# Kernel tuning notes

Hardware: AMD Instinct MI355X
Metric: run time of the kernel (lower is better)

## Reference

```python
import jax, jax.numpy as jnp
import numpy as np

T = 512   # timesteps (also used as batch-index count for packing)
B = 512   # batch (must equal T for this module's packing to be consistent)
D = 300   # state_dim
H = 128   # hidden_state_dim
E = 64    # embedding_dim
EGO = 12  # ego_state slice fed to the LSTMCell


def setup_inputs() -> dict:
    key = jax.random.key(0)
    ks = jax.random.split(key, 10)
    k = float(1.0 / np.sqrt(H))  # torch LSTMCell uniform init bound
    state = jax.random.normal(ks[0], (T, B, D), dtype=jnp.float32)
    hidden_state = jax.random.normal(ks[1], (B, H), dtype=jnp.float32) * 0.1
    cell_state = jax.random.normal(ks[2], (B, H), dtype=jnp.float32) * 0.1
    len_sequence = jax.random.randint(ks[3], (T,), 1, T + 1, dtype=jnp.int64 if jax.config.jax_enable_x64 else jnp.int32)
    W_ih = jax.random.uniform(ks[4], (4 * H, EGO), minval=-k, maxval=k, dtype=jnp.float32)
    W_hh = jax.random.uniform(ks[5], (4 * H, H), minval=-k, maxval=k, dtype=jnp.float32)
    b_ih = jax.random.uniform(ks[6], (4 * H,), minval=-k, maxval=k, dtype=jnp.float32)
    b_hh = jax.random.uniform(ks[7], (4 * H,), minval=-k, maxval=k, dtype=jnp.float32)
    W_emb = jax.random.normal(ks[8], (E, D + H), dtype=jnp.float32) * 0.05
    b_emb = jnp.zeros((E,), dtype=jnp.float32)
    return dict(state=state, hidden_state=hidden_state, cell_state=cell_state,
                len_sequence=len_sequence, W_ih=W_ih, W_hh=W_hh, b_ih=b_ih,
                b_hh=b_hh, W_emb=W_emb, b_emb=b_emb)


def _pack_indices(L):
    # tmp_output[t][:L[t]] concat over t -> flat indices into [T*B, .] (row-major t,b)
    idx_rnn = np.concatenate([t * B + np.arange(int(L[t])) for t in range(T)]) if T else np.zeros((0,), np.int32)
    # state.permute(1,0,2)[b][:L[b]] concat over b -> flat indices into [B*T, .] (row-major b,t)
    idx_state = np.concatenate([b * T + np.arange(int(L[b])) for b in range(B)]) if B else np.zeros((0,), np.int32)
    return jnp.asarray(idx_rnn, jnp.int32), jnp.asarray(idx_state, jnp.int32)


def _lstm_scan(x_seq, h0, c0, W_ih, W_hh, b_ih, b_hh):
    # torch.nn.LSTMCell math; gate order [i, f, g, o]
    def step(carry, x_t):
        h, c = carry
        gates = x_t @ W_ih.T + b_ih + h @ W_hh.T + b_hh  # [B, 4H]
        i, f, g, o = jnp.split(gates, 4, axis=-1)
        c_new = jax.nn.sigmoid(f) * c + jax.nn.sigmoid(i) * jnp.tanh(g)
        h_new = jax.nn.sigmoid(o) * jnp.tanh(c_new)
        return (h_new, c_new), h_new
    _, hs = jax.lax.scan(step, (h0, c0), x_seq)
    return hs  # [T, B, H]


def reference(state, hidden_state, cell_state, len_sequence, W_ih, W_hh, b_ih, b_hh, W_emb, b_emb):
    L = np.asarray(len_sequence)
    idx_rnn, idx_state = _pack_indices(L)
    rnn_input = state[:, :, :EGO]                               # [T, B, 12]
    hs = _lstm_scan(rnn_input, hidden_state, cell_state, W_ih, W_hh, b_ih, b_hh)  # [T, B, H]
    rnn_packed = hs.reshape(T * B, H)[idx_rnn]                  # [N, H]
    state_packed = jnp.transpose(state, (1, 0, 2)).reshape(B * T, D)[idx_state]  # [N, D]
    feats = jnp.concatenate([state_packed, rnn_packed], axis=1)  # [N, D+H]
    return feats @ W_emb.T + b_emb                               # [N, E]
```

## Files before the change

### kernel.cpp

```cpp
#include <hip/hip_runtime.h>
#include <hip/hip_fp16.h>

#define T_ 512
#define B_ 512
#define D_ 300
#define H_ 128
#define E_ 64
#define EGO_ 12
#define DH_ 428
#define BD_ 153600

typedef __attribute__((ext_vector_type(2))) _Float16 half2_t;
typedef __attribute__((ext_vector_type(8))) _Float16 half8_t;
typedef __attribute__((ext_vector_type(4))) float float4_t;

__device__ __forceinline__ unsigned pack2(float a, float b) {
  __half2 h = __floats2half2_rn(a, b);
  return __builtin_bit_cast(unsigned, h);
}
__device__ __forceinline__ half8_t h8(uint4 u) {
  return __builtin_bit_cast(half8_t, u);
}
__device__ __forceinline__ float sigm(float x) {
  float e = __builtin_amdgcn_exp2f(-1.4426950408889634f * x);
  return __builtin_amdgcn_rcpf(1.0f + e);
}
__device__ __forceinline__ float tanh_(float x) {
  float e = __builtin_amdgcn_exp2f(2.8853900817779268f * x);
  return 1.0f - 2.0f * __builtin_amdgcn_rcpf(1.0f + e);
}

__global__ void prefix_k(const int* __restrict__ L, int* __restrict__ pfx) {
  __shared__ int s[T_];
  int t = threadIdx.x;
  s[t] = L[t];
  __syncthreads();
  for (int off = 1; off < T_; off <<= 1) {
    int v = 0;
    if (t >= off) v = s[t - off];
    __syncthreads();
    s[t] += v;
    __syncthreads();
  }
  if (t == 0) pfx[0] = 0;
  pfx[t + 1] = s[t];
}

#define WS_ 84
__launch_bounds__(256, 1)
__global__ void scan_k(const float* __restrict__ state,
                       const float* __restrict__ h0,
                       const float* __restrict__ c0,
                       const int* __restrict__ lens,
                       const float* __restrict__ W_ih,
                       const float* __restrict__ W_hh,
                       const float* __restrict__ b_ih,
                       const float* __restrict__ b_hh,
                       const float* __restrict__ W_emb,
                       const float* __restrict__ b_emb,
                       const int* __restrict__ pfx,
                       float* __restrict__ out) {
  __shared__ __align__(16) unsigned hb[2][16][WS_];
  __shared__ int pfx_s[T_], len_s[T_];

  const int tid  = threadIdx.x;
  const int lane = tid & 63;
  const int w    = tid >> 6;
  const int n16  = lane & 15;
  const int quad = lane >> 4;
  const int b0   = blockIdx.x * 2;

  uint4 bfr[4][2][5];
  float bias[4][2];
#pragma unroll
  for (int c = 0; c < 4; ++c) {
#pragma unroll
    for (int p = 0; p < 2; ++p) {
      const int g = c * 128 + w * 32 + 2 * n16 + p;
      bias[c][p] = b_ih[g] + b_hh[g];
#pragma unroll
      for (int s = 0; s < 5; ++s) {
        unsigned pk[4];
#pragma unroll
        for (int pp = 0; pp < 4; ++pp) {
          const int k0 = s * 32 + quad * 8 + 2 * pp;
          float f0 = 0.f, f1 = 0.f;
          if (k0 < 128) { f0 = W_hh[g * H_ + k0]; f1 = W_hh[g * H_ + k0 + 1]; }
          else if (k0 < 140) {
            f0 = W_ih[g * EGO_ + (k0 - 128)];
            if (k0 + 1 < 140) f1 = W_ih[g * EGO_ + (k0 - 127)];
          }
          pk[pp] = pack2(f0, f1);
        }
        bfr[c][p][s] = make_uint4(pk[0], pk[1], pk[2], pk[3]);
      }
    }
  }
  uint4 efr[4];
  const int e_ = w * 16 + n16;
  const float bemb = b_emb[e_];
#pragma unroll
  for (int s = 0; s < 4; ++s) {
    unsigned pk[4];
#pragma unroll
    for (int pp = 0; pp < 4; ++pp) {
      const int k0 = s * 32 + quad * 8 + 2 * pp;
      pk[pp] = pack2(W_emb[e_ * DH_ + D_ + k0], W_emb[e_ * DH_ + D_ + k0 + 1]);
    }
    efr[s] = make_uint4(pk[0], pk[1], pk[2], pk[3]);
  }

  for (int i = tid; i < 2 * 16 * WS_; i += 256) ((unsigned*)hb)[i] = 0u;
  for (int i = tid; i < T_; i += 256) { pfx_s[i] = pfx[i]; len_s[i] = lens[i]; }
  __syncthreads();
  if (tid < 128) {
    const int r = tid >> 6, d = tid & 63;
    float2 v = ((const float2*)(h0 + (b0 + r) * H_))[d];
    hb[0][4 * r][d] = pack2(v.x, v.y);
  }
  float2 xheld = make_float2(0.f, 0.f);
  if (tid >= 16 && tid < 28) {
    const int j = tid - 16, row = j / 6, jj = j % 6;
    float2 v = ((const float2*)(state + (b0 + row) * D_))[jj];
    hb[0][4 * row][64 + jj] = pack2(v.x, v.y);
    xheld = ((const float2*)(state + BD_ + (b0 + row) * D_))[jj];
  }
  float cst[2] = {0.f, 0.f};
  if (quad < 2) {
#pragma unroll
    for (int p = 0; p < 2; ++p)
      cst[p] = c0[(b0 + quad) * H_ + w * 32 + 2 * n16 + p];
  }
  __syncthreads();

#pragma unroll 1
  for (int t = 0; t < T_; ++t) {
    const int pb = t & 1;
    float2 xnew = xheld;
    if (tid >= 16 && tid < 28) {
      const int j = tid - 16, row = j / 6, jj = j % 6;
      const int ttx = (t + 2 < T_) ? t + 2 : T_ - 1;
      xnew = ((const float2*)(state + (size_t)ttx * BD_ + (b0 + row) * D_))[jj];
    }

    uint4 a[5];
#pragma unroll
    for (int s = 0; s < 5; ++s)
      a[s] = *(const uint4*)(&hb[pb][n16][s * 16 + quad * 4]);

    if (t > 0) {
      float4_t ea = (float4_t){bemb, bemb, bemb, bemb};
#pragma unroll
      for (int s = 0; s < 4; ++s)
        ea = __builtin_amdgcn_mfma_f32_16x16x32_f16(h8(a[s]), h8(efr[s]), ea, 0, 0, 0);
      if (quad < 2) {
        const int Lt = len_s[t - 1];
        if (b0 + quad < Lt)
          out[((size_t)pfx_s[t - 1] + b0 + quad) * E_ + e_] = ea[0];
      }
    }

    float4_t acc[4][2];
#pragma unroll
    for (int c = 0; c < 4; ++c)
#pragma unroll
      for (int p = 0; p < 2; ++p)
        acc[c][p] = (float4_t){bias[c][p], bias[c][p], bias[c][p], bias[c][p]};
#pragma unroll
    for (int s = 0; s < 5; ++s) {
      const half8_t ah = h8(a[s]);
#pragma unroll
      for (int c = 0; c < 4; ++c)
#pragma unroll
        for (int p = 0; p < 2; ++p)
          acc[c][p] = __builtin_amdgcn_mfma_f32_16x16x32_f16(ah, h8(bfr[c][p][s]), acc[c][p], 0, 0, 0);
    }

    if (quad < 2) {
      float hp[2];
#pragma unroll
      for (int p = 0; p < 2; ++p) {
        const float gi = acc[0][p][0];
        const float gf = acc[1][p][0];
        const float gg = acc[2][p][0];
        const float go = acc[3][p][0];
        const float cc = sigm(gf) * cst[p] + sigm(gi) * tanh_(gg);
        cst[p] = cc;
        hp[p] = sigm(go) * tanh_(cc);
      }
      hb[1 - pb][quad * 4][w * 16 + n16] = pack2(hp[0], hp[1]);
    }
    if (tid >= 16 && tid < 28) {
      const int j = tid - 16, row = j / 6, jj = j % 6;
      hb[1 - pb][4 * row][64 + jj] = pack2(xheld.x, xheld.y);
      xheld = xnew;
    }
    __syncthreads();
  }

  {
    float4_t ea = (float4_t){bemb, bemb, bemb, bemb};
#pragma unroll
    for (int s = 0; s < 4; ++s) {
      uint4 a = *(const uint4*)(&hb[0][n16][s * 16 + quad * 4]);
      ea = __builtin_amdgcn_mfma_f32_16x16x32_f16(h8(a), h8(efr[s]), ea, 0, 0, 0);
    }
    if (quad < 2) {
      const int Lt = len_s[T_ - 1];
      if (b0 + quad < Lt)
        out[((size_t)pfx_s[T_ - 1] + b0 + quad) * E_ + e_] = ea[0];
    }
  }
}

#define ER_ 16
__launch_bounds__(256, 3)
__global__ void emb_state_k(const float* __restrict__ state,
                            const float* __restrict__ W_emb,
                            const int* __restrict__ pfx,
                            float* __restrict__ out, int N) {
  __shared__ int pfx_s[T_ + 1];

  const int tid  = threadIdx.x;
  const int lane = tid & 63;
  const int w    = tid >> 6;
  const int n16  = lane & 15;
  const int quad = lane >> 4;

  for (int i = tid; i <= T_; i += 256) pfx_s[i] = pfx[i];

  uint4 efr[10];
  const int e_ = w * 16 + n16;
#pragma unroll
  for (int s = 0; s < 10; ++s) {
    unsigned pk[4];
#pragma unroll
    for (int pp = 0; pp < 4; ++pp) {
      const int k0 = s * 32 + quad * 8 + 2 * pp;
      float f0 = 0.f, f1 = 0.f;
      if (k0 < D_) {
        f0 = W_emb[e_ * DH_ + k0];
        if (k0 + 1 < D_) f1 = W_emb[e_ * DH_ + k0 + 1];
      }
      pk[pp] = pack2(f0, f1);
    }
    efr[s] = make_uint4(pk[0], pk[1], pk[2], pk[3]);
  }
  __syncthreads();

  const int ntiles = (N + ER_ - 1) / ER_;
  for (int tile = blockIdx.x; tile < ntiles; tile += gridDim.x) {
    const int r0 = tile * ER_;
    int rA = r0 + n16;
    if (rA > N - 1) rA = N - 1;
    int lo = 0, hi = T_;
#pragma unroll
    for (int it = 0; it < 9; ++it) {
      const int mid = (lo + hi) >> 1;
      if (pfx_s[mid] <= rA) lo = mid; else hi = mid;
    }
    const float4* sp4 =
        (const float4*)(state + ((size_t)(rA - pfx_s[lo]) * B_ + lo) * D_) + quad * 2;

    float4 a0[10], a1[10];
#pragma unroll
    for (int s = 0; s < 9; ++s) { a0[s] = sp4[8 * s]; a1[s] = sp4[8 * s + 1]; }
    {
      const float4 z = make_float4(0.f, 0.f, 0.f, 0.f);
      a0[9] = (quad < 2) ? sp4[72] : z;
      a1[9] = (quad == 0) ? sp4[73] : z;
    }

    float4_t acc0 = (float4_t){0.f, 0.f, 0.f, 0.f};
    float4_t acc1 = (float4_t){0.f, 0.f, 0.f, 0.f};
#pragma unroll
    for (int s = 0; s < 10; ++s) {
      uint4 ua;
      ua.x = pack2(a0[s].x, a0[s].y);
      ua.y = pack2(a0[s].z, a0[s].w);
      ua.z = pack2(a1[s].x, a1[s].y);
      ua.w = pack2(a1[s].z, a1[s].w);
      if (s & 1) acc1 = __builtin_amdgcn_mfma_f32_16x16x32_f16(h8(ua), h8(efr[s]), acc1, 0, 0, 0);
      else       acc0 = __builtin_amdgcn_mfma_f32_16x16x32_f16(h8(ua), h8(efr[s]), acc0, 0, 0, 0);
    }
#pragma unroll
    for (int r = 0; r < 4; ++r) {
      const int R = r0 + quad * 4 + r;
      if (R < N) out[(size_t)R * E_ + e_] += acc0[r] + acc1[r];
    }
  }
}

extern "C" void kernel_launch(void* const* d_in, const int* in_sizes, int n_in,
                              void* d_out, int out_size, void* d_ws, size_t ws_size,
                              hipStream_t stream) {
  const float* state = (const float*)d_in[0];
  const float* h0    = (const float*)d_in[1];
  const float* c0    = (const float*)d_in[2];
  const int*   lens  = (const int*)d_in[3];
  const float* W_ih  = (const float*)d_in[4];
  const float* W_hh  = (const float*)d_in[5];
  const float* b_ih  = (const float*)d_in[6];
  const float* b_hh  = (const float*)d_in[7];
  const float* W_emb = (const float*)d_in[8];
  const float* b_emb = (const float*)d_in[9];
  float* out = (float*)d_out;
  int* pfx = (int*)d_ws;
  const int N = out_size / E_;

  prefix_k<<<1, T_, 0, stream>>>(lens, pfx);
  scan_k<<<B_ / 2, 256, 0, stream>>>(state, h0, c0, lens, W_ih, W_hh, b_ih, b_hh,
                                     W_emb, b_emb, pfx, out);
  const int ntiles = (N + ER_ - 1) / ER_;
  const int g = ntiles < 768 ? ntiles : 768;
  emb_state_k<<<g, 256, 0, stream>>>(state, W_emb, pfx, out, N);
}
```

Before: 835.2 us.

## Fuse state-embedding GEMM into the LSTM scan kernel and drop separate pass

Removes the separate emb_state_k kernel and computes the state part of the embedding inside the recurrent scan loop. Each step prefetches the packed state row for the block's two batch indices into a double-buffered shared tile and runs extra MFMAs alongside the hidden-state embedding, writing the full output once. This removes a second kernel launch, the read-modify-write of the output, and the binary search for the packing, but adds work and latency to the serial per-timestep critical path and more register pressure (10 extra fragment registers).

```diff
diff --git a/kernel.cpp b/kernel.cpp
--- a/kernel.cpp
+++ b/kernel.cpp
@@ -47,6 +47,7 @@
 }
 
 #define WS_ 84
+#define SST_ 160
 __launch_bounds__(256, 1)
 __global__ void scan_k(const float* __restrict__ state,
                        const float* __restrict__ h0,
@@ -61,6 +62,7 @@
                        const int* __restrict__ pfx,
                        float* __restrict__ out) {
   __shared__ __align__(16) unsigned hb[2][16][WS_];
+  __shared__ __align__(16) unsigned sst[2][3][SST_];
   __shared__ int pfx_s[T_], len_s[T_];
 
   const int tid  = threadIdx.x;
@@ -96,7 +98,7 @@
       }
     }
   }
-  uint4 efr[4];
+  uint4 efr[4], sfr[10];
   const int e_ = w * 16 + n16;
   const float bemb = b_emb[e_];
 #pragma unroll
@@ -109,8 +111,21 @@
     }
     efr[s] = make_uint4(pk[0], pk[1], pk[2], pk[3]);
   }
+#pragma unroll
+  for (int s = 0; s < 10; ++s) {
+    unsigned pk[4];
+#pragma unroll
+    for (int pp = 0; pp < 4; ++pp) {
+      const int k0 = s * 32 + quad * 8 + 2 * pp;
+      float f0 = 0.f, f1 = 0.f;
+      if (k0 < D_) { f0 = W_emb[e_ * DH_ + k0]; f1 = W_emb[e_ * DH_ + k0 + 1]; }
+      pk[pp] = pack2(f0, f1);
+    }
+    sfr[s] = make_uint4(pk[0], pk[1], pk[2], pk[3]);
+  }
 
   for (int i = tid; i < 2 * 16 * WS_; i += 256) ((unsigned*)hb)[i] = 0u;
+  for (int i = tid; i < 2 * 3 * SST_; i += 256) ((unsigned*)sst)[i] = 0u;
   for (int i = tid; i < T_; i += 256) { pfx_s[i] = pfx[i]; len_s[i] = lens[i]; }
   __syncthreads();
   if (tid < 128) {
@@ -125,6 +140,16 @@
     hb[0][4 * row][64 + jj] = pack2(v.x, v.y);
     xheld = ((const float2*)(state + BD_ + (b0 + row) * D_))[jj];
   }
+  int srow_r = 0, s_i = 0;
+  size_t sbase = 0;
+  float4 sheld = make_float4(0.f, 0.f, 0.f, 0.f);
+  if (tid < 150) {
+    srow_r = tid / 75; s_i = tid % 75;
+    sbase = (size_t)(b0 + srow_r) * B_ * D_ + 4 * s_i;
+    if (b0 + srow_r < len_s[0])
+      sheld = *(const float4*)(state + sbase);
+  }
+  const int rsel = (n16 == 0) ? 0 : ((n16 == 4) ? 1 : 2);
   float cst[2] = {0.f, 0.f};
   if (quad < 2) {
 #pragma unroll
@@ -142,6 +167,12 @@
       const int ttx = (t + 2 < T_) ? t + 2 : T_ - 1;
       xnew = ((const float2*)(state + (size_t)ttx * BD_ + (b0 + row) * D_))[jj];
     }
+    float4 snew = sheld;
+    if (tid < 150) {
+      const int tts = (t + 1 < T_) ? t + 1 : T_ - 1;
+      if (b0 + srow_r < len_s[tts])
+        snew = *(const float4*)(state + sbase + (size_t)tts * D_);
+    }
 
     uint4 a[5];
 #pragma unroll
@@ -149,14 +180,27 @@
       a[s] = *(const uint4*)(&hb[pb][n16][s * 16 + quad * 4]);
 
     if (t > 0) {
-      float4_t ea = (float4_t){bemb, bemb, bemb, bemb};
-#pragma unroll
-      for (int s = 0; s < 4; ++s)
-        ea = __builtin_amdgcn_mfma_f32_16x16x32_f16(h8(a[s]), h8(efr[s]), ea, 0, 0, 0);
-      if (quad < 2) {
-        const int Lt = len_s[t - 1];
-        if (b0 + quad < Lt)
-          out[((size_t)pfx_s[t - 1] + b0 + quad) * E_ + e_] = ea[0];
+      const int Lt = len_s[t - 1];
+      if (b0 < Lt) {
+        float4_t er  = (float4_t){bemb, bemb, bemb, bemb};
+        float4_t es0 = (float4_t){0.f, 0.f, 0.f, 0.f};
+        float4_t es1 = (float4_t){0.f, 0.f, 0.f, 0.f};
+#pragma unroll
+        for (int s = 0; s < 4; ++s)
+          er = __builtin_amdgcn_mfma_f32_16x16x32_f16(h8(a[s]), h8(efr[s]), er, 0, 0, 0);
+        const unsigned* sb = &sst[pb][rsel][0];
+#pragma unroll
+        for (int s = 0; s < 5; ++s) {
+          uint4 sa = *(const uint4*)(sb + s * 16 + quad * 4);
+          es0 = __builtin_amdgcn_mfma_f32_16x16x32_f16(h8(sa), h8(sfr[s]), es0, 0, 0, 0);
+        }
+#pragma unroll
+        for (int s = 5; s < 10; ++s) {
+          uint4 sa = *(const uint4*)(sb + s * 16 + quad * 4);
+          es1 = __builtin_amdgcn_mfma_f32_16x16x32_f16(h8(sa), h8(sfr[s]), es1, 0, 0, 0);
+        }
+        if (quad < 2 && b0 + quad < Lt)
+          out[((size_t)pfx_s[t - 1] + b0 + quad) * E_ + e_] = er[0] + es0[0] + es1[0];
       }
     }
 
@@ -195,98 +239,39 @@
       hb[1 - pb][4 * row][64 + jj] = pack2(xheld.x, xheld.y);
       xheld = xnew;
     }
+    if (tid < 150) {
+      unsigned* d = &sst[1 - pb][srow_r][2 * s_i];
+      d[0] = pack2(sheld.x, sheld.y);
+      d[1] = pack2(sheld.z, sheld.w);
+      sheld = snew;
+    }
     __syncthreads();
   }
 
   {
-    float4_t ea = (float4_t){bemb, bemb, bemb, bemb};
-#pragma unroll
-    for (int s = 0; s < 4; ++s) {
-      uint4 a = *(const uint4*)(&hb[0][n16][s * 16 + quad * 4]);
-      ea = __builtin_amdgcn_mfma_f32_16x16x32_f16(h8(a), h8(efr[s]), ea, 0, 0, 0);
-    }
-    if (quad < 2) {
-      const int Lt = len_s[T_ - 1];
-      if (b0 + quad < Lt)
-        out[((size_t)pfx_s[T_ - 1] + b0 + quad) * E_ + e_] = ea[0];
-    }
-  }
-}
-
-#define ER_ 16
-__launch_bounds__(256, 3)
-__global__ void emb_state_k(const float* __restrict__ state,
-                            const float* __restrict__ W_emb,
-                            const int* __restrict__ pfx,
-                            float* __restrict__ out, int N) {
-  __shared__ int pfx_s[T_ + 1];
-
-  const int tid  = threadIdx.x;
-  const int lane = tid & 63;
-  const int w    = tid >> 6;
-  const int n16  = lane & 15;
-  const int quad = lane >> 4;
-
-  for (int i = tid; i <= T_; i += 256) pfx_s[i] = pfx[i];
-
-  uint4 efr[10];
-  const int e_ = w * 16 + n16;
-#pragma unroll
-  for (int s = 0; s < 10; ++s) {
-    unsigned pk[4];
-#pragma unroll
-    for (int pp = 0; pp < 4; ++pp) {
-      const int k0 = s * 32 + quad * 8 + 2 * pp;
-      float f0 = 0.f, f1 = 0.f;
-      if (k0 < D_) {
-        f0 = W_emb[e_ * DH_ + k0];
-        if (k0 + 1 < D_) f1 = W_emb[e_ * DH_ + k0 + 1];
-      }
-      pk[pp] = pack2(f0, f1);
-    }
-    efr[s] = make_uint4(pk[0], pk[1], pk[2], pk[3]);
-  }
-  __syncthreads();
-
-  const int ntiles = (N + ER_ - 1) / ER_;
-  for (int tile = blockIdx.x; tile < ntiles; tile += gridDim.x) {
-    const int r0 = tile * ER_;
-    int rA = r0 + n16;
-    if (rA > N - 1) rA = N - 1;
-    int lo = 0, hi = T_;
-#pragma unroll
-    for (int it = 0; it < 9; ++it) {
-      const int mid = (lo + hi) >> 1;
-      if (pfx_s[mid] <= rA) lo = mid; else hi = mid;
-    }
-    const float4* sp4 =
-        (const float4*)(state + ((size_t)(rA - pfx_s[lo]) * B_ + lo) * D_) + quad * 2;
-
-    float4 a0[10], a1[10];
-#pragma unroll
-    for (int s = 0; s < 9; ++s) { a0[s] = sp4[8 * s]; a1[s] = sp4[8 * s + 1]; }
-    {
-      const float4 z = make_float4(0.f, 0.f, 0.f, 0.f);
-      a0[9] = (quad < 2) ? sp4[72] : z;
-      a1[9] = (quad == 0) ? sp4[73] : z;
-    }
-
-    float4_t acc0 = (float4_t){0.f, 0.f, 0.f, 0.f};
-    float4_t acc1 = (float4_t){0.f, 0.f, 0.f, 0.f};
-#pragma unroll
-    for (int s = 0; s < 10; ++s) {
-      uint4 ua;
-      ua.x = pack2(a0[s].x, a0[s].y);
-      ua.y = pack2(a0[s].z, a0[s].w);
-      ua.z = pack2(a1[s].x, a1[s].y);
-      ua.w = pack2(a1[s].z, a1[s].w);
-      if (s & 1) acc1 = __builtin_amdgcn_mfma_f32_16x16x32_f16(h8(ua), h8(efr[s]), acc1, 0, 0, 0);
-      else       acc0 = __builtin_amdgcn_mfma_f32_16x16x32_f16(h8(ua), h8(efr[s]), acc0, 0, 0, 0);
-    }
-#pragma unroll
-    for (int r = 0; r < 4; ++r) {
-      const int R = r0 + quad * 4 + r;
-      if (R < N) out[(size_t)R * E_ + e_] += acc0[r] + acc1[r];
+    const int Lt = len_s[T_ - 1];
+    if (b0 < Lt) {
+      float4_t er  = (float4_t){bemb, bemb, bemb, bemb};
+      float4_t es0 = (float4_t){0.f, 0.f, 0.f, 0.f};
+      float4_t es1 = (float4_t){0.f, 0.f, 0.f, 0.f};
+#pragma unroll
+      for (int s = 0; s < 4; ++s) {
+        uint4 a = *(const uint4*)(&hb[0][n16][s * 16 + quad * 4]);
+        er = __builtin_amdgcn_mfma_f32_16x16x32_f16(h8(a), h8(efr[s]), er, 0, 0, 0);
+      }
+      const unsigned* sb = &sst[0][rsel][0];
+#pragma unroll
+      for (int s = 0; s < 5; ++s) {
+        uint4 sa = *(const uint4*)(sb + s * 16 + quad * 4);
+        es0 = __builtin_amdgcn_mfma_f32_16x16x32_f16(h8(sa), h8(sfr[s]), es0, 0, 0, 0);
+      }
+#pragma unroll
+      for (int s = 5; s < 10; ++s) {
+        uint4 sa = *(const uint4*)(sb + s * 16 + quad * 4);
+        es1 = __builtin_amdgcn_mfma_f32_16x16x32_f16(h8(sa), h8(sfr[s]), es1, 0, 0, 0);
+      }
+      if (quad < 2 && b0 + quad < Lt)
+        out[((size_t)pfx_s[T_ - 1] + b0 + quad) * E_ + e_] = er[0] + es0[0] + es1[0];
     }
   }
 }
@@ -306,12 +291,8 @@
   const float* b_emb = (const float*)d_in[9];
   float* out = (float*)d_out;
   int* pfx = (int*)d_ws;
-  const int N = out_size / E_;
 
   prefix_k<<<1, T_, 0, stream>>>(lens, pfx);
   scan_k<<<B_ / 2, 256, 0, stream>>>(state, h0, c0, lens, W_ih, W_hh, b_ih, b_hh,
                                      W_emb, b_emb, pfx, out);
-  const int ntiles = (N + ER_ - 1) / ER_;
-  const int g = ntiles < 768 ? ntiles : 768;
-  emb_state_k<<<g, 256, 0, stream>>>(state, W_emb, pfx, out, N);
-}
+}
```

After: 941.6 us. +12.7%, slower.
